# Kernel optimization log

Hardware: AMD Instinct MI355X
Metric: run time of the kernel (lower is better)

Reference implementation:

```python
import jax, jax.numpy as jnp
import numpy as np

B, T, D, H = 16, 81, 128, 8  # batch, ntok, d_model (= d_head), n_head


def setup_inputs() -> dict:
    key = jax.random.key(0)
    ks = jax.random.split(key, 6)
    s = 0.02
    return {
        "x": jax.random.normal(ks[0], (B, T, D), jnp.float32),
        "msk": jnp.ones((1, H, T, T), jnp.float32),
        "wqkv_w": jax.random.normal(ks[1], (H * 2 * D, D), jnp.float32) * s,
        "wqkv_b": jax.random.normal(ks[2], (H * 2 * D,), jnp.float32) * s,
        "wk_w": jax.random.normal(ks[3], (H, D), jnp.float32) * s,
        "fanout_w": jax.random.normal(ks[4], (D, D), jnp.float32) * s,
        "fanout_b": jax.random.normal(ks[5], (D,), jnp.float32) * s,
        "head_enabled": jnp.ones((H,), jnp.float32),
        "n": 0, "layer": 0, "pas": 1,
    }


def quick_gelu(x):
    return x * jax.nn.sigmoid(1.702 * x)


def reference(x, msk, wqkv_w, wqkv_b, wk_w, fanout_w, fanout_b, head_enabled, n, layer, pas):
    b, t, d = x.shape
    h = wk_w.shape[0]
    # qkv projection: per-head q and v of full width d (d_head == d_model)
    y = x @ wqkv_w.T + wqkv_b                      # [b, t, h*2*d]
    y = y.reshape(b, t, h, 2 * d)
    q, v = y[..., :d], y[..., d:]                  # [b, t, h, d] each
    # k: input gated per-head by wk.weight rows
    k = x[:, :, None, :] * wk_w[None, None, :, :]  # [b, t, h, d]
    # v gating by head-enabled flags
    v = v * head_enabled[None, None, :, None]
    # L1 attention scores: a[b,h,t,s] = -sum_d |q[b,t,h,d] - k[b,s,h,d]| / sqrt(d)
    diff = jnp.abs(q[:, :, None, :, :] - k[:, None, :, :, :])  # [b, t, s, h, d]
    a = -diff.sum(-1)                               # [b, t, s, h]
    a = jnp.transpose(a, (0, 3, 1, 2)) / jnp.sqrt(jnp.asarray(d, x.dtype))  # [b,h,t,s]
    a = jax.nn.softmax(a, axis=3) * msk
    bo = jnp.einsum('bhts,bshd->bthd', a, v)        # [b, t, h, d]
    bo = bo.sum(axis=2)                             # sum over heads -> [b, t, d]
    ap = jnp.transpose(a[0] - 1.0 + msk[0], (1, 2, 0))  # [t, s, h]
    z = quick_gelu(bo + 4.0) - 4.0
    z = z @ fanout_w.T + fanout_b
    return (x + z, ap)
```

## Files before the change

### kernel.cpp

```cpp
#include <hip/hip_runtime.h>
#include <math.h>

#define Bq 16
#define Tq 81
#define Dq 128
#define Hq 8
#define BT (Bq*Tq)
#define BTD (Bq*Tq*Dq)
#define PS 84
#define P_SZ   (Bq*Tq*Hq*PS)
#define QV_SZ  (BT*Hq*Dq)
#define P_OFF  0
#define Q_OFF  (P_OFF + P_SZ)
#define V_OFF  (Q_OFF + QV_SZ)

#define LSTR 136

#define TCH 3
#define NCH 27

typedef __attribute__((ext_vector_type(8))) short short8;
typedef __attribute__((ext_vector_type(4))) float f32x4;

__device__ __forceinline__ float l1_4(const float4 q, const float4 k) {
    return fabsf(q.x - k.x) + fabsf(q.y - k.y) + fabsf(q.z - k.z) + fabsf(q.w - k.w);
}
__device__ __forceinline__ int imin(int a, int b) { return a < b ? a : b; }
__device__ __forceinline__ unsigned short f2bf(float f) {
    unsigned u = __float_as_uint(f);
    u += 0x7fffu + ((u >> 16) & 1u);
    return (unsigned short)(u >> 16);
}
__device__ __forceinline__ float bf2f(unsigned short s) {
    return __uint_as_float((unsigned)s << 16);
}

__global__ __launch_bounds__(256) void k_qkv_mfma(
    const float* __restrict__ x, const float* __restrict__ wqkv,
    const float* __restrict__ bias, const float* __restrict__ he,
    float* __restrict__ Qo, unsigned short* __restrict__ Vb)
{
    __shared__ unsigned short xs[64 * LSTR];
    __shared__ unsigned short wsh[64 * LSTR];
    const int tid = threadIdx.x;
    const int w = tid >> 6, lane = tid & 63;
    const int ln = lane & 15, quad = lane >> 4;
    const int r0 = blockIdx.x * 64;
    const int n0 = blockIdx.y * 64;
    const int h  = blockIdx.y >> 2;
    const int isV = (blockIdx.y >> 1) & 1;
    const int c0 = (blockIdx.y & 1) * 64;

    #pragma unroll
    for (int i = 0; i < 8; ++i) {
        const int idx = tid + i * 256;
        const int r = idx >> 5, c4 = idx & 31;
        const int gr = imin(r0 + r, BT - 1);
        const float4 v = *(const float4*)(x + (size_t)gr * Dq + c4 * 4);
        ushort4 o;
        o.x = f2bf(v.x); o.y = f2bf(v.y); o.z = f2bf(v.z); o.w = f2bf(v.w);
        *(ushort4*)(&xs[r * LSTR + c4 * 4]) = o;

        const float4 vw = *(const float4*)(wqkv + (size_t)(n0 + r) * Dq + c4 * 4);
        ushort4 ow;
        ow.x = f2bf(vw.x); ow.y = f2bf(vw.y); ow.z = f2bf(vw.z); ow.w = f2bf(vw.w);
        *(ushort4*)(&wsh[r * LSTR + c4 * 4]) = ow;
    }
    __syncthreads();

    const unsigned short* xa = xs + (w * 16 + ln) * LSTR + quad * 8;
    const unsigned short* wb = wsh + ln * LSTR + quad * 8;

    f32x4 acc[4];
    #pragma unroll
    for (int i = 0; i < 4; ++i) acc[i] = (f32x4){0.f, 0.f, 0.f, 0.f};

    #pragma unroll
    for (int kb = 0; kb < Dq; kb += 32) {
        const short8 af = *(const short8*)(xa + kb);
        #pragma unroll
        for (int nt = 0; nt < 4; ++nt) {
            const short8 bf = *(const short8*)(wb + nt * 16 * LSTR + kb);
            acc[nt] = __builtin_amdgcn_mfma_f32_16x16x32_bf16(af, bf, acc[nt], 0, 0, 0);
        }
    }

    const float scale = isV ? he[h] : 1.0f;
    const int gm0 = r0 + w * 16 + quad * 4;
    #pragma unroll
    for (int nt = 0; nt < 4; ++nt) {
        const float bn = bias[n0 + nt * 16 + ln];
        #pragma unroll
        for (int r = 0; r < 4; ++r) {
            const int gm = gm0 + r;
            if (gm < BT) {
                const int bb = gm / 81, tt = gm - bb * 81;
                const size_t o =
                    (((size_t)bb * Hq + h) * Tq + tt) * Dq + c0 + nt * 16 + ln;
                const float val = (acc[nt][r] + bn) * scale;
                if (isV) Vb[o] = f2bf(val);
                else     Qo[o] = val;
            }
        }
    }
}

__global__ __launch_bounds__(512) void k_attn_out(
    const float* __restrict__ x, const float* __restrict__ Q,
    const float* __restrict__ wk, const float* __restrict__ msk,
    const unsigned short* __restrict__ Vb, const float* __restrict__ fw,
    const float* __restrict__ fb, float* __restrict__ out)
{
    __shared__ float smem[14464];
    __shared__ float Pl[Hq][TCH][PS];
    float* const xl  = smem;
    float* const Ql  = smem + 10368;
    float* const wkl = smem + 13440;
    float* const bo  = smem;
    float* const zs  = smem + 4096;

    const int tid = threadIdx.x;
    const int t0 = blockIdx.x * TCH, b = blockIdx.y;
    const int w = tid >> 6, lane = tid & 63;

    for (int idx = tid; idx < Tq * 32; idx += 512) {
        const int r = idx >> 5, g = idx & 31;
        const float4 v = *(const float4*)(x + (size_t)(b * Tq + r) * Dq + g * 4);
        *(float4*)(&xl[r * Dq + ((g ^ (r & 7)) << 2)]) = v;
    }
    for (int idx = tid; idx < Hq * TCH * 32; idx += 512) {
        const int row = idx >> 5, g = idx & 31;
        const int h = row / TCH, i = row - h * TCH;
        const float4 v =
            *(const float4*)(Q + (((size_t)b * Hq + h) * Tq + t0 + i) * Dq + g * 4);
        *(float4*)(&Ql[row * Dq + g * 4]) = v;
    }
    if (tid < 256) {
        const float4 v = *(const float4*)(wk + tid * 4);
        *(float4*)(&wkl[tid * 4]) = v;
    }
    __syncthreads();

    const float* wkw = wkl + w * Dq;
    const float* qb  = Ql + w * TCH * Dq;
    float acc0[TCH];
    #pragma unroll
    for (int i = 0; i < TCH; ++i) acc0[i] = 0.f;
    {
        const int s = lane;
        #pragma unroll 2
        for (int g = 0; g < 32; ++g) {
            const float4 wv = *(const float4*)(wkw + g * 4);
            float4 k0 = *(const float4*)(&xl[s * Dq + ((g ^ (s & 7)) << 2)]);
            k0.x *= wv.x; k0.y *= wv.y; k0.z *= wv.z; k0.w *= wv.w;
            #pragma unroll
            for (int i = 0; i < TCH; ++i) {
                const float4 qv = *(const float4*)(qb + i * Dq + g * 4);
                acc0[i] += l1_4(qv, k0);
            }
        }
    }
    const float ns = -0.08838834764831845f;
    {
        if (lane < TCH * 17) {
            const int tt = lane / 17, j = lane - tt * 17;
            const int s = 64 + j;
            float a = 0.f;
            #pragma unroll 2
            for (int g = 0; g < 32; ++g) {
                const float4 wv = *(const float4*)(wkw + g * 4);
                float4 kv = *(const float4*)(&xl[s * Dq + ((g ^ (s & 7)) << 2)]);
                kv.x *= wv.x; kv.y *= wv.y; kv.z *= wv.z; kv.w *= wv.w;
                const float4 qv = *(const float4*)(qb + tt * Dq + g * 4);
                a += l1_4(qv, kv);
            }
            Pl[w][tt][s] = a * ns;
        }
    }
    __syncthreads();

    {
        const bool has1 = (lane < Tq - 64);
        const int s1 = 64 + lane;
        #pragma unroll
        for (int i = 0; i < TCH; ++i) {
            const float v0 = acc0[i] * ns;
            const float v1 = has1 ? Pl[w][i][s1] : -1e30f;
            float m = fmaxf(v0, v1);
            #pragma unroll
            for (int off = 32; off > 0; off >>= 1)
                m = fmaxf(m, __shfl_xor(m, off));
            const float e0 = __expf(v0 - m);
            const float e1 = has1 ? __expf(v1 - m) : 0.f;
            float ssum = e0 + e1;
            #pragma unroll
            for (int off = 32; off > 0; off >>= 1)
                ssum += __shfl_xor(ssum, off);
            const float rinv = 1.0f / ssum;
            const float* mrow = msk + ((size_t)w * Tq + (t0 + i)) * Tq;
            const float mv0 = mrow[lane];
            const float p0 = e0 * rinv * mv0;
            Pl[w][i][lane] = p0;
            if (b == 0)
                out[BTD + ((size_t)(t0 + i) * Tq + lane) * Hq + w] = p0 - 1.0f + mv0;
            if (has1) {
                const float mv1 = mrow[s1];
                const float p1 = e1 * rinv * mv1;
                Pl[w][i][s1] = p1;
                if (b == 0)
                    out[BTD + ((size_t)(t0 + i) * Tq + s1) * Hq + w] = p1 - 1.0f + mv1;
            }
        }
    }
    __syncthreads();

    {
        const int d0 = lane * 2;
        float2 acc[TCH];
        #pragma unroll
        for (int i = 0; i < TCH; ++i) acc[i] = make_float2(0.f, 0.f);
        const unsigned short* vp = Vb + (((size_t)b * Hq + w) * Tq) * Dq + d0;
        for (int s4 = 0; s4 < 20; ++s4) {
            float4 p[TCH];
            #pragma unroll
            for (int t = 0; t < TCH; ++t)
                p[t] = *(const float4*)(&Pl[w][t][s4 * 4]);
            #pragma unroll
            for (int ss = 0; ss < 4; ++ss) {
                const int s = s4 * 4 + ss;
                const ushort2 uv = *(const ushort2*)(vp + (size_t)s * Dq);
                const float vx = bf2f(uv.x), vy = bf2f(uv.y);
                #pragma unroll
                for (int t = 0; t < TCH; ++t) {
                    const float pv = ((const float*)&p[t])[ss];
                    acc[t].x = fmaf(pv, vx, acc[t].x);
                    acc[t].y = fmaf(pv, vy, acc[t].y);
                }
            }
        }
        {
            const ushort2 uv = *(const ushort2*)(vp + (size_t)80 * Dq);
            const float vx = bf2f(uv.x), vy = bf2f(uv.y);
            #pragma unroll
            for (int t = 0; t < TCH; ++t) {
                const float pv = Pl[w][t][80];
                acc[t].x = fmaf(pv, vx, acc[t].x);
                acc[t].y = fmaf(pv, vy, acc[t].y);
            }
        }
        #pragma unroll
        for (int t = 0; t < TCH; ++t) {
            bo[(w * TCH + t) * Dq + d0]     = acc[t].x;
            bo[(w * TCH + t) * Dq + d0 + 1] = acc[t].y;
        }
    }
    __syncthreads();

    for (int idx = tid; idx < TCH * Dq; idx += 512) {
        const int t = idx >> 7, d = idx & 127;
        float s = 0.f;
        #pragma unroll
        for (int ww = 0; ww < 8; ++ww) s += bo[(ww * TCH + t) * Dq + d];
        const float tt2 = s + 4.0f;
        const float sg = 1.0f / (1.0f + __expf(-1.702f * tt2));
        zs[t * Dq + d] = tt2 * sg - 4.0f;
    }
    __syncthreads();

    {
        const int n = tid & 127, tg = tid >> 7;
        if (tg < TCH) {
            const float* fwr = fw + (size_t)n * Dq;
            float a0 = 0.f;
            #pragma unroll 8
            for (int k4 = 0; k4 < 32; ++k4) {
                const float4 w4 = *(const float4*)(fwr + k4 * 4);
                const float4 z0 = *(const float4*)(&zs[tg * Dq + k4 * 4]);
                a0 += z0.x * w4.x + z0.y * w4.y + z0.z * w4.z + z0.w * w4.w;
            }
            const size_t o = ((size_t)b * Tq + t0 + tg) * Dq + n;
            out[o] = x[o] + a0 + fb[n];
        }
    }
}

extern "C" void kernel_launch(void* const* d_in, const int* in_sizes, int n_in,
                              void* d_out, int out_size, void* d_ws, size_t ws_size,
                              hipStream_t stream) {
    const float* x        = (const float*)d_in[0];
    const float* msk      = (const float*)d_in[1];
    const float* wqkv_w   = (const float*)d_in[2];
    const float* wqkv_b   = (const float*)d_in[3];
    const float* wk_w     = (const float*)d_in[4];
    const float* fanout_w = (const float*)d_in[5];
    const float* fanout_b = (const float*)d_in[6];
    const float* he       = (const float*)d_in[7];
    float* out = (float*)d_out;
    float* ws  = (float*)d_ws;

    float* Q  = ws + Q_OFF;
    unsigned short* Vb = (unsigned short*)(ws + V_OFF);

    k_qkv_mfma<<<dim3(21, 32), 256, 0, stream>>>(x, wqkv_w, wqkv_b, he, Q, Vb);
    k_attn_out<<<dim3(NCH, 16), 512, 0, stream>>>(x, Q, wk_w, msk, Vb,
                                                  fanout_w, fanout_b, out);
}
```

Baseline: 114.8 us.

## Read Q and wk via uniform scalar loads and split PV across half-waves

Drops the LDS staging of Q and wk. Each wave now reads them from global memory through pointers made wave-uniform with readfirstlane, so the compiler can use scalar loads. This removes one staging pass and a block barrier, and the barrier between score computation and softmax is also removed. The P·V loop is reworked so each half-wave covers half of the key positions with 4-wide bf16 loads, and the halves are combined with a cross-lane shuffle. The probability row is zero-padded to 84 entries so the last chunk reads V rows past the end of each head's slice, which could run out of bounds at the final (batch, head) or meet non-finite values there.

```diff
diff --git a/kernel.cpp b/kernel.cpp
--- a/kernel.cpp
+++ b/kernel.cpp
@@ -33,6 +33,12 @@
 }
 __device__ __forceinline__ float bf2f(unsigned short s) {
     return __uint_as_float((unsigned)s << 16);
+}
+__device__ __forceinline__ const float* rfl_ptr(const float* p) {
+    unsigned long long u = (unsigned long long)p;
+    const unsigned lo = __builtin_amdgcn_readfirstlane((unsigned)u);
+    const unsigned hi = __builtin_amdgcn_readfirstlane((unsigned)(u >> 32));
+    return (const float*)(((unsigned long long)hi << 32) | lo);
 }
 
 __global__ __launch_bounds__(256) void k_qkv_mfma(
@@ -111,11 +117,9 @@
     const unsigned short* __restrict__ Vb, const float* __restrict__ fw,
     const float* __restrict__ fb, float* __restrict__ out)
 {
-    __shared__ float smem[14464];
+    __shared__ float smem[10368];
     __shared__ float Pl[Hq][TCH][PS];
     float* const xl  = smem;
-    float* const Ql  = smem + 10368;
-    float* const wkl = smem + 13440;
     float* const bo  = smem;
     float* const zs  = smem + 4096;
 
@@ -128,21 +132,11 @@
         const float4 v = *(const float4*)(x + (size_t)(b * Tq + r) * Dq + g * 4);
         *(float4*)(&xl[r * Dq + ((g ^ (r & 7)) << 2)]) = v;
     }
-    for (int idx = tid; idx < Hq * TCH * 32; idx += 512) {
-        const int row = idx >> 5, g = idx & 31;
-        const int h = row / TCH, i = row - h * TCH;
-        const float4 v =
-            *(const float4*)(Q + (((size_t)b * Hq + h) * Tq + t0 + i) * Dq + g * 4);
-        *(float4*)(&Ql[row * Dq + g * 4]) = v;
-    }
-    if (tid < 256) {
-        const float4 v = *(const float4*)(wk + tid * 4);
-        *(float4*)(&wkl[tid * 4]) = v;
-    }
-    __syncthreads();
-
-    const float* wkw = wkl + w * Dq;
-    const float* qb  = Ql + w * TCH * Dq;
+    __syncthreads();
+
+    const float* wku = rfl_ptr(wk + (size_t)w * Dq);
+    const float* qbu = rfl_ptr(Q + (((size_t)b * Hq + w) * Tq + t0) * Dq);
+
     float acc0[TCH];
     #pragma unroll
     for (int i = 0; i < TCH; ++i) acc0[i] = 0.f;
@@ -150,12 +144,12 @@
         const int s = lane;
         #pragma unroll 2
         for (int g = 0; g < 32; ++g) {
-            const float4 wv = *(const float4*)(wkw + g * 4);
+            const float4 wv = *(const float4*)(wku + g * 4);
             float4 k0 = *(const float4*)(&xl[s * Dq + ((g ^ (s & 7)) << 2)]);
             k0.x *= wv.x; k0.y *= wv.y; k0.z *= wv.z; k0.w *= wv.w;
             #pragma unroll
             for (int i = 0; i < TCH; ++i) {
-                const float4 qv = *(const float4*)(qb + i * Dq + g * 4);
+                const float4 qv = *(const float4*)(qbu + i * Dq + g * 4);
                 acc0[i] += l1_4(qv, k0);
             }
         }
@@ -168,16 +162,15 @@
             float a = 0.f;
             #pragma unroll 2
             for (int g = 0; g < 32; ++g) {
-                const float4 wv = *(const float4*)(wkw + g * 4);
+                const float4 wv = *(const float4*)(wku + g * 4);
                 float4 kv = *(const float4*)(&xl[s * Dq + ((g ^ (s & 7)) << 2)]);
                 kv.x *= wv.x; kv.y *= wv.y; kv.z *= wv.z; kv.w *= wv.w;
-                const float4 qv = *(const float4*)(qb + tt * Dq + g * 4);
+                const float4 qv = *(const float4*)(qbu + tt * Dq + g * 4);
                 a += l1_4(qv, kv);
             }
             Pl[w][tt][s] = a * ns;
         }
     }
-    __syncthreads();
 
     {
         const bool has1 = (lane < Tq - 64);
@@ -210,48 +203,53 @@
                 if (b == 0)
                     out[BTD + ((size_t)(t0 + i) * Tq + s1) * Hq + w] = p1 - 1.0f + mv1;
             }
-        }
-    }
-    __syncthreads();
-
-    {
-        const int d0 = lane * 2;
-        float2 acc[TCH];
-        #pragma unroll
-        for (int i = 0; i < TCH; ++i) acc[i] = make_float2(0.f, 0.f);
+            if (lane < 3) Pl[w][i][81 + lane] = 0.f;
+        }
+    }
+    __syncthreads();
+
+    {
+        const int d2 = lane & 31, sh = lane >> 5;
+        const int d0 = d2 * 4;
         const unsigned short* vp = Vb + (((size_t)b * Hq + w) * Tq) * Dq + d0;
-        for (int s4 = 0; s4 < 20; ++s4) {
+        float4 acc[TCH];
+        #pragma unroll
+        for (int t = 0; t < TCH; ++t) acc[t] = make_float4(0.f, 0.f, 0.f, 0.f);
+        const int sb = sh * 44;
+        const int nck = 11 - sh;
+        for (int c = 0; c < nck; ++c) {
+            const int s0c = sb + c * 4;
             float4 p[TCH];
             #pragma unroll
             for (int t = 0; t < TCH; ++t)
-                p[t] = *(const float4*)(&Pl[w][t][s4 * 4]);
+                p[t] = *(const float4*)(&Pl[w][t][s0c]);
             #pragma unroll
             for (int ss = 0; ss < 4; ++ss) {
-                const int s = s4 * 4 + ss;
-                const ushort2 uv = *(const ushort2*)(vp + (size_t)s * Dq);
+                const int s = s0c + ss;
+                const ushort4 uv = *(const ushort4*)(vp + (size_t)s * Dq);
                 const float vx = bf2f(uv.x), vy = bf2f(uv.y);
+                const float vz = bf2f(uv.z), vw2 = bf2f(uv.w);
                 #pragma unroll
                 for (int t = 0; t < TCH; ++t) {
                     const float pv = ((const float*)&p[t])[ss];
-                    acc[t].x = fmaf(pv, vx, acc[t].x);
-                    acc[t].y = fmaf(pv, vy, acc[t].y);
+                    acc[t].x = fmaf(pv, vx,  acc[t].x);
+                    acc[t].y = fmaf(pv, vy,  acc[t].y);
+                    acc[t].z = fmaf(pv, vz,  acc[t].z);
+                    acc[t].w = fmaf(pv, vw2, acc[t].w);
                 }
             }
         }
-        {
-            const ushort2 uv = *(const ushort2*)(vp + (size_t)80 * Dq);
-            const float vx = bf2f(uv.x), vy = bf2f(uv.y);
-            #pragma unroll
-            for (int t = 0; t < TCH; ++t) {
-                const float pv = Pl[w][t][80];
-                acc[t].x = fmaf(pv, vx, acc[t].x);
-                acc[t].y = fmaf(pv, vy, acc[t].y);
-            }
-        }
         #pragma unroll
         for (int t = 0; t < TCH; ++t) {
-            bo[(w * TCH + t) * Dq + d0]     = acc[t].x;
-            bo[(w * TCH + t) * Dq + d0 + 1] = acc[t].y;
+            acc[t].x += __shfl_xor(acc[t].x, 32);
+            acc[t].y += __shfl_xor(acc[t].y, 32);
+            acc[t].z += __shfl_xor(acc[t].z, 32);
+            acc[t].w += __shfl_xor(acc[t].w, 32);
+        }
+        if (sh == 0) {
+            #pragma unroll
+            for (int t = 0; t < TCH; ++t)
+                *(float4*)(&bo[(w * TCH + t) * Dq + d0]) = acc[t];
         }
     }
     __syncthreads();
```

New measurement: 127.4 us. 11.0% more time.

## Compute L1 attention scores in packed fp16 with one query row per block

Applied to the files above, without the earlier changes.

The L1 score computation now converts x, Q and wk to fp16 in shared memory and uses packed half subtract/multiply plus a dot2 instruction to sum absolute differences. The attention kernel also drops from three query rows per block to one, launching 81x16 blocks instead of 27x16. This roughly halves score ALU work and shared memory footprint and adds parallelism. In exchange each block reloads x, V and fanout weights, so global traffic rises, and fp16 precision may loosen the accuracy of scores and softmax.

```diff
diff --git a/kernel.cpp b/kernel.cpp
--- a/kernel.cpp
+++ b/kernel.cpp
@@ -16,15 +16,10 @@
 
 #define LSTR 136
 
-#define TCH 3
-#define NCH 27
-
 typedef __attribute__((ext_vector_type(8))) short short8;
 typedef __attribute__((ext_vector_type(4))) float f32x4;
-
-__device__ __forceinline__ float l1_4(const float4 q, const float4 k) {
-    return fabsf(q.x - k.x) + fabsf(q.y - k.y) + fabsf(q.z - k.z) + fabsf(q.w - k.w);
-}
+typedef _Float16 h2 __attribute__((ext_vector_type(2)));
+
 __device__ __forceinline__ int imin(int a, int b) { return a < b ? a : b; }
 __device__ __forceinline__ unsigned short f2bf(float f) {
     unsigned u = __float_as_uint(f);
@@ -33,6 +28,21 @@
 }
 __device__ __forceinline__ float bf2f(unsigned short s) {
     return __uint_as_float((unsigned)s << 16);
+}
+__device__ __forceinline__ unsigned pk2h(float a, float b) {
+    h2 v; v[0] = (_Float16)a; v[1] = (_Float16)b;
+    return *(unsigned*)&v;
+}
+__device__ __forceinline__ float l1h(unsigned qv, unsigned xv, unsigned wv, float acc) {
+    const h2 q = *(const h2*)&qv, xx = *(const h2*)&xv, ww = *(const h2*)&wv;
+    h2 d = q - xx * ww;
+    unsigned du = (*(unsigned*)&d) & 0x7fff7fffu;
+    const h2 da = *(const h2*)&du;
+#if __has_builtin(__builtin_amdgcn_fdot2)
+    return __builtin_amdgcn_fdot2(da, (h2){(_Float16)1.f, (_Float16)1.f}, acc, false);
+#else
+    return acc + (float)da[0] + (float)da[1];
+#endif
 }
 
 __global__ __launch_bounds__(256) void k_qkv_mfma(
@@ -111,176 +121,162 @@
     const unsigned short* __restrict__ Vb, const float* __restrict__ fw,
     const float* __restrict__ fb, float* __restrict__ out)
 {
-    __shared__ float smem[14464];
-    __shared__ float Pl[Hq][TCH][PS];
-    float* const xl  = smem;
-    float* const Ql  = smem + 10368;
-    float* const wkl = smem + 13440;
-    float* const bo  = smem;
-    float* const zs  = smem + 4096;
+    __shared__ unsigned short xlh[Tq * Dq];
+    __shared__ unsigned short Qlh[Hq * Dq];
+    __shared__ unsigned short wklh[Hq * Dq];
+    __shared__ float Pl[Hq][PS];
+    float* const bo = (float*)xlh;
+    float* const zs = (float*)xlh + 1024;
 
     const int tid = threadIdx.x;
-    const int t0 = blockIdx.x * TCH, b = blockIdx.y;
+    const int t0 = blockIdx.x, b = blockIdx.y;
     const int w = tid >> 6, lane = tid & 63;
 
-    for (int idx = tid; idx < Tq * 32; idx += 512) {
-        const int r = idx >> 5, g = idx & 31;
-        const float4 v = *(const float4*)(x + (size_t)(b * Tq + r) * Dq + g * 4);
-        *(float4*)(&xl[r * Dq + ((g ^ (r & 7)) << 2)]) = v;
-    }
-    for (int idx = tid; idx < Hq * TCH * 32; idx += 512) {
-        const int row = idx >> 5, g = idx & 31;
-        const int h = row / TCH, i = row - h * TCH;
-        const float4 v =
-            *(const float4*)(Q + (((size_t)b * Hq + h) * Tq + t0 + i) * Dq + g * 4);
-        *(float4*)(&Ql[row * Dq + g * 4]) = v;
-    }
-    if (tid < 256) {
-        const float4 v = *(const float4*)(wk + tid * 4);
-        *(float4*)(&wkl[tid * 4]) = v;
-    }
-    __syncthreads();
-
-    const float* wkw = wkl + w * Dq;
-    const float* qb  = Ql + w * TCH * Dq;
-    float acc0[TCH];
-    #pragma unroll
-    for (int i = 0; i < TCH; ++i) acc0[i] = 0.f;
+    for (int idx = tid; idx < Tq * 16; idx += 512) {
+        const int r = idx >> 4, g8 = idx & 15;
+        const float* src = x + (size_t)(b * Tq + r) * Dq + g8 * 8;
+        const float4 a = *(const float4*)(src);
+        const float4 c = *(const float4*)(src + 4);
+        uint4 o;
+        o.x = pk2h(a.x, a.y); o.y = pk2h(a.z, a.w);
+        o.z = pk2h(c.x, c.y); o.w = pk2h(c.z, c.w);
+        *(uint4*)(&xlh[r * Dq + ((g8 ^ (r & 7)) << 3)]) = o;
+    }
+    if (tid < 128) {
+        const int hh = tid >> 4, g8 = tid & 15;
+        const float* src = Q + (((size_t)b * Hq + hh) * Tq + t0) * Dq + g8 * 8;
+        const float4 a = *(const float4*)(src);
+        const float4 c = *(const float4*)(src + 4);
+        uint4 o;
+        o.x = pk2h(a.x, a.y); o.y = pk2h(a.z, a.w);
+        o.z = pk2h(c.x, c.y); o.w = pk2h(c.z, c.w);
+        *(uint4*)(&Qlh[hh * Dq + g8 * 8]) = o;
+    }
+    if (tid >= 256 && tid < 384) {
+        const int t2 = tid - 256;
+        const int hh = t2 >> 4, g8 = t2 & 15;
+        const float* src = wk + (size_t)hh * Dq + g8 * 8;
+        const float4 a = *(const float4*)(src);
+        const float4 c = *(const float4*)(src + 4);
+        uint4 o;
+        o.x = pk2h(a.x, a.y); o.y = pk2h(a.z, a.w);
+        o.z = pk2h(c.x, c.y); o.w = pk2h(c.z, c.w);
+        *(uint4*)(&wklh[hh * Dq + g8 * 8]) = o;
+    }
+    __syncthreads();
+
+    const unsigned short* wrow = wklh + w * Dq;
+    const unsigned short* qrow = Qlh + w * Dq;
+    const int sx = (lane & 7) << 3;
+    float acc0 = 0.f, acc1 = 0.f;
     {
-        const int s = lane;
-        #pragma unroll 2
-        for (int g = 0; g < 32; ++g) {
-            const float4 wv = *(const float4*)(wkw + g * 4);
-            float4 k0 = *(const float4*)(&xl[s * Dq + ((g ^ (s & 7)) << 2)]);
-            k0.x *= wv.x; k0.y *= wv.y; k0.z *= wv.z; k0.w *= wv.w;
-            #pragma unroll
-            for (int i = 0; i < TCH; ++i) {
-                const float4 qv = *(const float4*)(qb + i * Dq + g * 4);
-                acc0[i] += l1_4(qv, k0);
-            }
-        }
-    }
-    const float ns = -0.08838834764831845f;
+        const unsigned short* xrow = xlh + (size_t)lane * Dq;
+        #pragma unroll 4
+        for (int g8 = 0; g8 < 16; ++g8) {
+            const uint4 kk = *(const uint4*)(xrow + ((g8 << 3) ^ sx));
+            const uint4 wv = *(const uint4*)(wrow + (g8 << 3));
+            const uint4 qq = *(const uint4*)(qrow + (g8 << 3));
+            acc0 = l1h(qq.x, kk.x, wv.x, acc0);
+            acc0 = l1h(qq.y, kk.y, wv.y, acc0);
+            acc0 = l1h(qq.z, kk.z, wv.z, acc0);
+            acc0 = l1h(qq.w, kk.w, wv.w, acc0);
+        }
+    }
+    if (lane < Tq - 64) {
+        const unsigned short* xrow = xlh + (size_t)(64 + lane) * Dq;
+        #pragma unroll 4
+        for (int g8 = 0; g8 < 16; ++g8) {
+            const uint4 kk = *(const uint4*)(xrow + ((g8 << 3) ^ sx));
+            const uint4 wv = *(const uint4*)(wrow + (g8 << 3));
+            const uint4 qq = *(const uint4*)(qrow + (g8 << 3));
+            acc1 = l1h(qq.x, kk.x, wv.x, acc1);
+            acc1 = l1h(qq.y, kk.y, wv.y, acc1);
+            acc1 = l1h(qq.z, kk.z, wv.z, acc1);
+            acc1 = l1h(qq.w, kk.w, wv.w, acc1);
+        }
+    }
+
     {
-        if (lane < TCH * 17) {
-            const int tt = lane / 17, j = lane - tt * 17;
-            const int s = 64 + j;
-            float a = 0.f;
-            #pragma unroll 2
-            for (int g = 0; g < 32; ++g) {
-                const float4 wv = *(const float4*)(wkw + g * 4);
-                float4 kv = *(const float4*)(&xl[s * Dq + ((g ^ (s & 7)) << 2)]);
-                kv.x *= wv.x; kv.y *= wv.y; kv.z *= wv.z; kv.w *= wv.w;
-                const float4 qv = *(const float4*)(qb + tt * Dq + g * 4);
-                a += l1_4(qv, kv);
-            }
-            Pl[w][tt][s] = a * ns;
-        }
-    }
-    __syncthreads();
-
-    {
+        const float ns = -0.08838834764831845f;
         const bool has1 = (lane < Tq - 64);
-        const int s1 = 64 + lane;
-        #pragma unroll
-        for (int i = 0; i < TCH; ++i) {
-            const float v0 = acc0[i] * ns;
-            const float v1 = has1 ? Pl[w][i][s1] : -1e30f;
-            float m = fmaxf(v0, v1);
-            #pragma unroll
-            for (int off = 32; off > 0; off >>= 1)
-                m = fmaxf(m, __shfl_xor(m, off));
-            const float e0 = __expf(v0 - m);
-            const float e1 = has1 ? __expf(v1 - m) : 0.f;
-            float ssum = e0 + e1;
-            #pragma unroll
-            for (int off = 32; off > 0; off >>= 1)
-                ssum += __shfl_xor(ssum, off);
-            const float rinv = 1.0f / ssum;
-            const float* mrow = msk + ((size_t)w * Tq + (t0 + i)) * Tq;
-            const float mv0 = mrow[lane];
-            const float p0 = e0 * rinv * mv0;
-            Pl[w][i][lane] = p0;
+        const float v0 = acc0 * ns;
+        const float v1 = has1 ? acc1 * ns : -1e30f;
+        float m = fmaxf(v0, v1);
+        #pragma unroll
+        for (int off = 32; off > 0; off >>= 1)
+            m = fmaxf(m, __shfl_xor(m, off));
+        const float e0 = __expf(v0 - m);
+        const float e1 = has1 ? __expf(v1 - m) : 0.f;
+        float ssum = e0 + e1;
+        #pragma unroll
+        for (int off = 32; off > 0; off >>= 1)
+            ssum += __shfl_xor(ssum, off);
+        const float rinv = 1.0f / ssum;
+        const float* mrow = msk + ((size_t)w * Tq + t0) * Tq;
+        const float mv0 = mrow[lane];
+        const float p0 = e0 * rinv * mv0;
+        Pl[w][lane] = p0;
+        if (b == 0)
+            out[BTD + ((size_t)t0 * Tq + lane) * Hq + w] = p0 - 1.0f + mv0;
+        if (has1) {
+            const float mv1 = mrow[64 + lane];
+            const float p1 = e1 * rinv * mv1;
+            Pl[w][64 + lane] = p1;
             if (b == 0)
-                out[BTD + ((size_t)(t0 + i) * Tq + lane) * Hq + w] = p0 - 1.0f + mv0;
-            if (has1) {
-                const float mv1 = mrow[s1];
-                const float p1 = e1 * rinv * mv1;
-                Pl[w][i][s1] = p1;
-                if (b == 0)
-                    out[BTD + ((size_t)(t0 + i) * Tq + s1) * Hq + w] = p1 - 1.0f + mv1;
-            }
-        }
+                out[BTD + ((size_t)t0 * Tq + 64 + lane) * Hq + w] = p1 - 1.0f + mv1;
+        }
+        if (lane < 3) Pl[w][81 + lane] = 0.f;
     }
     __syncthreads();
 
     {
         const int d0 = lane * 2;
-        float2 acc[TCH];
-        #pragma unroll
-        for (int i = 0; i < TCH; ++i) acc[i] = make_float2(0.f, 0.f);
+        float2 acc = make_float2(0.f, 0.f);
         const unsigned short* vp = Vb + (((size_t)b * Hq + w) * Tq) * Dq + d0;
         for (int s4 = 0; s4 < 20; ++s4) {
-            float4 p[TCH];
-            #pragma unroll
-            for (int t = 0; t < TCH; ++t)
-                p[t] = *(const float4*)(&Pl[w][t][s4 * 4]);
+            const float4 p = *(const float4*)(&Pl[w][s4 * 4]);
             #pragma unroll
             for (int ss = 0; ss < 4; ++ss) {
                 const int s = s4 * 4 + ss;
                 const ushort2 uv = *(const ushort2*)(vp + (size_t)s * Dq);
-                const float vx = bf2f(uv.x), vy = bf2f(uv.y);
-                #pragma unroll
-                for (int t = 0; t < TCH; ++t) {
-                    const float pv = ((const float*)&p[t])[ss];
-                    acc[t].x = fmaf(pv, vx, acc[t].x);
-                    acc[t].y = fmaf(pv, vy, acc[t].y);
-                }
+                const float pv = ((const float*)&p)[ss];
+                acc.x = fmaf(pv, bf2f(uv.x), acc.x);
+                acc.y = fmaf(pv, bf2f(uv.y), acc.y);
             }
         }
         {
             const ushort2 uv = *(const ushort2*)(vp + (size_t)80 * Dq);
-            const float vx = bf2f(uv.x), vy = bf2f(uv.y);
-            #pragma unroll
-            for (int t = 0; t < TCH; ++t) {
-                const float pv = Pl[w][t][80];
-                acc[t].x = fmaf(pv, vx, acc[t].x);
-                acc[t].y = fmaf(pv, vy, acc[t].y);
-            }
-        }
-        #pragma unroll
-        for (int t = 0; t < TCH; ++t) {
-            bo[(w * TCH + t) * Dq + d0]     = acc[t].x;
-            bo[(w * TCH + t) * Dq + d0 + 1] = acc[t].y;
-        }
-    }
-    __syncthreads();
-
-    for (int idx = tid; idx < TCH * Dq; idx += 512) {
-        const int t = idx >> 7, d = idx & 127;
+            const float pv = Pl[w][80];
+            acc.x = fmaf(pv, bf2f(uv.x), acc.x);
+            acc.y = fmaf(pv, bf2f(uv.y), acc.y);
+        }
+        bo[w * Dq + d0]     = acc.x;
+        bo[w * Dq + d0 + 1] = acc.y;
+    }
+    __syncthreads();
+
+    if (tid < Dq) {
         float s = 0.f;
         #pragma unroll
-        for (int ww = 0; ww < 8; ++ww) s += bo[(ww * TCH + t) * Dq + d];
+        for (int ww = 0; ww < 8; ++ww) s += bo[ww * Dq + tid];
         const float tt2 = s + 4.0f;
         const float sg = 1.0f / (1.0f + __expf(-1.702f * tt2));
-        zs[t * Dq + d] = tt2 * sg - 4.0f;
-    }
-    __syncthreads();
-
-    {
-        const int n = tid & 127, tg = tid >> 7;
-        if (tg < TCH) {
-            const float* fwr = fw + (size_t)n * Dq;
-            float a0 = 0.f;
-            #pragma unroll 8
-            for (int k4 = 0; k4 < 32; ++k4) {
-                const float4 w4 = *(const float4*)(fwr + k4 * 4);
-                const float4 z0 = *(const float4*)(&zs[tg * Dq + k4 * 4]);
-                a0 += z0.x * w4.x + z0.y * w4.y + z0.z * w4.z + z0.w * w4.w;
-            }
-            const size_t o = ((size_t)b * Tq + t0 + tg) * Dq + n;
-            out[o] = x[o] + a0 + fb[n];
-        }
+        zs[tid] = tt2 * sg - 4.0f;
+    }
+    __syncthreads();
+
+    if (tid < Dq) {
+        const int n = tid;
+        const float* fwr = fw + (size_t)n * Dq;
+        float a0 = 0.f;
+        #pragma unroll 8
+        for (int k4 = 0; k4 < 32; ++k4) {
+            const float4 w4 = *(const float4*)(fwr + k4 * 4);
+            const float4 z0 = *(const float4*)(&zs[k4 * 4]);
+            a0 += z0.x * w4.x + z0.y * w4.y + z0.z * w4.z + z0.w * w4.w;
+        }
+        const size_t o = ((size_t)b * Tq + t0) * Dq + n;
+        out[o] = x[o] + a0 + fb[n];
     }
 }
 
@@ -302,6 +298,6 @@
     unsigned short* Vb = (unsigned short*)(ws + V_OFF);
 
     k_qkv_mfma<<<dim3(21, 32), 256, 0, stream>>>(x, wqkv_w, wqkv_b, he, Q, Vb);
-    k_attn_out<<<dim3(NCH, 16), 512, 0, stream>>>(x, Q, wk_w, msk, Vb,
-                                                  fanout_w, fanout_b, out);
-}
+    k_attn_out<<<dim3(Tq, 16), 512, 0, stream>>>(x, Q, wk_w, msk, Vb,
+                                                 fanout_w, fanout_b, out);
+}
```

Result: faster. 111.6 us, median of 2 (-2.7%).
